# Optimization experiments

Hardware: AMD Instinct MI355X
Metric: run time of the kernel (lower is better)

## Reference

```python
import jax, jax.numpy as jnp
import numpy as np

N_TRIPLES = 2_000_000
IN_DIM = 128
FILTERS = 128
NUM_SEGMENTS = 100_000
LOG2 = 0.6931471805599453

def shifted_softplus(x):
    # softplus(x) - log(2), as in SchNet/CFnet
    return jax.nn.softplus(x) - LOG2

def setup_inputs() -> dict:
    key = jax.random.key(0)
    k1, k2, k3, k4 = jax.random.split(key, 4)
    dijk = jax.random.normal(k1, (N_TRIPLES, IN_DIM), dtype=jnp.float32)
    seg_j = jnp.sort(jax.random.randint(k2, (N_TRIPLES,), 0, NUM_SEGMENTS, dtype=jnp.int32))
    W1 = jax.random.normal(k3, (IN_DIM, FILTERS), dtype=jnp.float32) * (1.0 / np.sqrt(IN_DIM))
    b1 = jnp.zeros((FILTERS,), dtype=jnp.float32)
    W2 = jax.random.normal(k4, (FILTERS, FILTERS), dtype=jnp.float32) * (1.0 / np.sqrt(FILTERS))
    b2 = jnp.zeros((FILTERS,), dtype=jnp.float32)
    return {"dijk": dijk, "seg_j": seg_j, "W1": W1, "b1": b1, "W2": W2, "b2": b2}

def reference(dijk, seg_j, W1, b1, W2, b2):
    # dense1 + shifted softplus: [n, in] @ [in, f] -> [n, f]
    h = shifted_softplus(dijk @ W1 + b1)
    # dense2 + shifted softplus: [n, f] -> [n, f]
    w_ijk = shifted_softplus(h @ W2 + b2)
    # sum-pool over segments keyed by seg_j -> [num_segments, f]
    w_ij = jax.ops.segment_sum(w_ijk, seg_j, num_segments=NUM_SEGMENTS)
    return w_ij
```

## Files before the change

kernel.cpp:

```cpp
#include <hip/hip_runtime.h>
#include <hip/hip_bf16.h>
#include <cstdint>
#include <cstddef>


typedef float  f32x4  __attribute__((ext_vector_type(4)));
typedef __bf16 bf16x8 __attribute__((ext_vector_type(8)));

typedef uint32_t u32a    __attribute__((may_alias));
typedef bf16x8   bf16x8a __attribute__((may_alias));
typedef __bf16   bf16a   __attribute__((may_alias));

static constexpr int   N_TRIPLES = 2000000;
static constexpr int   DIM       = 128;
static constexpr int   NSEG      = 100000;
static constexpr int   ROWS      = 128;
static constexpr float LOG2F_    = 0.6931471805599453f;
static constexpr float LOG2E_    = 1.4426950408889634f;

__device__ __forceinline__ float sp2_(float y) {
  float t = __builtin_amdgcn_exp2f(-__builtin_fabsf(y));
  return fmaxf(y, 0.0f) + __builtin_amdgcn_logf(1.0f + t);
}

__global__ void wt_kernel(const float* __restrict__ W1, const float* __restrict__ W2,
                          __bf16* __restrict__ WT) {
  int t = blockIdx.x * 256 + threadIdx.x;
  int k = t >> 7;
  int n = t & 127;
  WT[n * 128 + k]         = (__bf16)(W1[t] * LOG2E_);
  WT[16384 + n * 128 + k] = (__bf16)W2[t];
}

__global__ void bias_kernel(const float* __restrict__ b1, const float* __restrict__ W2,
                            const float* __restrict__ b2,
                            float* __restrict__ b1p, float* __restrict__ b2p) {
  int n = threadIdx.x;
  float s = 0.0f;
  #pragma unroll 8
  for (int k = 0; k < 128; ++k) s += W2[k * 128 + n];
  b1p[n] = b1[n] * LOG2E_;
  b2p[n] = (b2[n] - LOG2F_ * s) * LOG2E_;
}

__global__ __launch_bounds__(512, 6) void fused_kernel(
    const float* __restrict__ dijk, const int* __restrict__ seg,
    const __bf16* __restrict__ WT,
    const float* __restrict__ b1v, const float* __restrict__ b2p,
    float* __restrict__ out)
{
  __shared__ __bf16 tile[ROWS * DIM];

  const int tid  = threadIdx.x;
  const int lane = tid & 63;
  const int wave = tid >> 6;
  const int l15  = lane & 15;
  const int g    = lane >> 4;
  const int r0   = blockIdx.x * ROWS;

  char* tb = (char*)tile;

  {
    int row = tid >> 2, q = tid & 3;
    const float* src = dijk + (size_t)(r0 + row) * DIM + q * 32;
    char* dst = tb + row * 256;
    int swz = (row & 7) << 4;
    #pragma unroll
    for (int u = 0; u < 4; ++u) {
      f32x4 v0 = *(const f32x4*)(src + u * 8);
      f32x4 v1 = *(const f32x4*)(src + u * 8 + 4);
      bf16x8 t8;
      t8[0] = (__bf16)v0[0]; t8[1] = (__bf16)v0[1]; t8[2] = (__bf16)v0[2]; t8[3] = (__bf16)v0[3];
      t8[4] = (__bf16)v1[0]; t8[5] = (__bf16)v1[1]; t8[6] = (__bf16)v1[2]; t8[7] = (__bf16)v1[3];
      *(bf16x8a*)(dst + ((q * 64 + u * 16) ^ swz)) = t8;
    }
  }

  const int colw = wave * 16 + l15;
  const float bias1 = b1v[colw];
  const float bias2 = b2p[colw];

  const int  swA = (l15 & 7) << 4;
  const char* abase = tb + l15 * 256;
  uint32_t bo[4];
  #pragma unroll
  for (int ks = 0; ks < 4; ++ks) bo[ks] = (uint32_t)((ks * 64 + g * 16) ^ swA);
  uint32_t wbase[4];
  #pragma unroll
  for (int j = 0; j < 4; ++j) {
    int rj = g * 4 + j;
    wbase[j] = (uint32_t)(rj * 256 + ((colw * 2) ^ ((rj & 7) << 4)));
  }

  __syncthreads();

  f32x4 acc[8];
  {
    bf16x8 bf1[4];
    #pragma unroll
    for (int ks = 0; ks < 4; ++ks)
      bf1[ks] = *(const bf16x8*)(WT + colw * 128 + ks * 32 + g * 8);

    #pragma unroll
    for (int mt = 0; mt < 8; ++mt) acc[mt] = (f32x4){0.f, 0.f, 0.f, 0.f};
    #pragma unroll
    for (int mt = 0; mt < 8; ++mt) {
      const char* pm = abase + mt * 4096;
      #pragma unroll
      for (int ks = 0; ks < 4; ++ks) {
        bf16x8 a = *(const bf16x8a*)(pm + bo[ks]);
        acc[mt] = __builtin_amdgcn_mfma_f32_16x16x32_bf16(a, bf1[ks], acc[mt], 0, 0, 0);
      }
    }
  }

  __syncthreads();

  #pragma unroll
  for (int mt = 0; mt < 8; ++mt) {
    #pragma unroll
    for (int j = 0; j < 4; ++j) {
      float u1 = sp2_(acc[mt][j] + bias1);
      *(bf16a*)(tb + wbase[j] + mt * 4096) = (__bf16)u1;
    }
  }

  __syncthreads();

  f32x4 acc2[8];
  {
    bf16x8 bf2[4];
    #pragma unroll
    for (int ks = 0; ks < 4; ++ks)
      bf2[ks] = *(const bf16x8*)(WT + 16384 + colw * 128 + ks * 32 + g * 8);

    #pragma unroll
    for (int mt = 0; mt < 8; ++mt) acc2[mt] = (f32x4){0.f, 0.f, 0.f, 0.f};
    #pragma unroll
    for (int mt = 0; mt < 8; ++mt) {
      const char* pm = abase + mt * 4096;
      #pragma unroll
      for (int ks = 0; ks < 4; ++ks) {
        bf16x8 a = *(const bf16x8a*)(pm + bo[ks]);
        acc2[mt] = __builtin_amdgcn_mfma_f32_16x16x32_bf16(a, bf2[ks], acc2[mt], 0, 0, 0);
      }
    }
  }

  __syncthreads();

  #pragma unroll
  for (int mt = 0; mt < 8; ++mt) {
    #pragma unroll
    for (int j = 0; j < 4; ++j) {
      float u2 = sp2_(acc2[mt][j] + bias2);
      float wv = __builtin_fmaf(u2, LOG2F_, -LOG2F_);
      *(bf16a*)(tb + wbase[j] + mt * 4096) = (__bf16)wv;
    }
  }

  __syncthreads();

  {
    const int colb = (tid & 63) * 2;
    const int hh   = tid >> 6;
    const int rbeg = hh * 16;
    const int* sp = seg + r0;
    const char* rp[8];
    #pragma unroll
    for (int k = 0; k < 8; ++k)
      rp[k] = tb + rbeg * 256 + ((colb * 2) ^ (k << 4));
    float a0 = 0.0f, a1 = 0.0f;
    int cur = sp[rbeg];
    #pragma unroll
    for (int i = 0; i < 16; ++i) {
      int s = sp[rbeg + i];
      if (s != cur) {
        atomicAdd(out + (size_t)cur * DIM + colb,     a0);
        atomicAdd(out + (size_t)cur * DIM + colb + 1, a1);
        a0 = 0.0f; a1 = 0.0f; cur = s;
      }
      uint32_t w = *(const u32a*)(rp[i & 7] + i * 256);
      a0 += __uint_as_float(w << 16);
      a1 += __uint_as_float(w & 0xffff0000u);
    }
    atomicAdd(out + (size_t)cur * DIM + colb,     a0);
    atomicAdd(out + (size_t)cur * DIM + colb + 1, a1);
  }
}

extern "C" void kernel_launch(void* const* d_in, const int* in_sizes, int n_in,
                              void* d_out, int out_size, void* d_ws, size_t ws_size,
                              hipStream_t stream) {
  const float* dijk = (const float*)d_in[0];
  const int*   seg  = (const int*)d_in[1];
  const float* W1   = (const float*)d_in[2];
  const float* b1   = (const float*)d_in[3];
  const float* W2   = (const float*)d_in[4];
  const float* b2   = (const float*)d_in[5];
  float* out = (float*)d_out;

  float*  b1p = (float*)d_ws;
  float*  b2p = (float*)((char*)d_ws + 512);
  __bf16* WT  = (__bf16*)((char*)d_ws + 1024);

  (void)hipMemsetAsync(out, 0, (size_t)NSEG * DIM * sizeof(float), stream);

  wt_kernel<<<64, 256, 0, stream>>>(W1, W2, WT);
  bias_kernel<<<1, 128, 0, stream>>>(b1, W2, b2, b1p, b2p);

  fused_kernel<<<N_TRIPLES / ROWS, 512, 0, stream>>>(dijk, seg, WT, b1p, b2p, out);
}
```

Before: 422.7 us.

## Split row tile into two halves and software-pipeline loads, GEMMs and activations

Splits the 128-row tile into two 64-row halves in shared memory. Each stage is interleaved across the halves: the second half's global load overlaps the first half's GEMM1, and each half's softplus epilogue overlaps the other half's MFMA work. The goal is to hide global-load latency and transcendental ALU time behind matrix instructions within one block. In exchange it adds two extra block barriers and reloads the W1 fragment, and register pressure may rise because several accumulator sets are live together.

After: 425.1 us. No clear change (+0.6%).

```diff
diff --git a/kernel.cpp b/kernel.cpp
--- a/kernel.cpp
+++ b/kernel.cpp
@@ -58,30 +58,24 @@
   const int g    = lane >> 4;
   const int r0   = blockIdx.x * ROWS;
 
-  char* tb = (char*)tile;
-
-  {
-    int row = tid >> 2, q = tid & 3;
-    const float* src = dijk + (size_t)(r0 + row) * DIM + q * 32;
-    char* dst = tb + row * 256;
-    int swz = (row & 7) << 4;
-    #pragma unroll
-    for (int u = 0; u < 4; ++u) {
-      f32x4 v0 = *(const f32x4*)(src + u * 8);
-      f32x4 v1 = *(const f32x4*)(src + u * 8 + 4);
-      bf16x8 t8;
-      t8[0] = (__bf16)v0[0]; t8[1] = (__bf16)v0[1]; t8[2] = (__bf16)v0[2]; t8[3] = (__bf16)v0[3];
-      t8[4] = (__bf16)v1[0]; t8[5] = (__bf16)v1[1]; t8[6] = (__bf16)v1[2]; t8[7] = (__bf16)v1[3];
-      *(bf16x8a*)(dst + ((q * 64 + u * 16) ^ swz)) = t8;
-    }
-  }
+  char* tA = (char*)tile;
+  char* tB = (char*)tile + 16384;
+
+  const int  srow = tid >> 3;
+  const int  soct = tid & 7;
+  const int  sswz = (srow & 7) << 4;
+  char* sdstA = tA + srow * 256;
+  char* sdstB = tB + srow * 256;
+  const uint32_t so0 = (uint32_t)((soct * 32)      ^ sswz);
+  const uint32_t so1 = (uint32_t)((soct * 32 + 16) ^ sswz);
+  const float* gsrcA = dijk + (size_t)(r0 + srow) * DIM + soct * 16;
+  const float* gsrcB = gsrcA + (size_t)64 * DIM;
 
   const int colw = wave * 16 + l15;
   const float bias1 = b1v[colw];
   const float bias2 = b2p[colw];
 
   const int  swA = (l15 & 7) << 4;
-  const char* abase = tb + l15 * 256;
   uint32_t bo[4];
   #pragma unroll
   for (int ks = 0; ks < 4; ++ks) bo[ks] = (uint32_t)((ks * 64 + g * 16) ^ swA);
@@ -92,84 +86,158 @@
     wbase[j] = (uint32_t)(rj * 256 + ((colw * 2) ^ ((rj & 7) << 4)));
   }
 
-  __syncthreads();
-
-  f32x4 acc[8];
-  {
+  {
+    f32x4 v0 = *(const f32x4*)(gsrcA);
+    f32x4 v1 = *(const f32x4*)(gsrcA + 4);
+    f32x4 v2 = *(const f32x4*)(gsrcA + 8);
+    f32x4 v3 = *(const f32x4*)(gsrcA + 12);
+    bf16x8 t8a, t8b;
+    t8a[0]=(__bf16)v0[0]; t8a[1]=(__bf16)v0[1]; t8a[2]=(__bf16)v0[2]; t8a[3]=(__bf16)v0[3];
+    t8a[4]=(__bf16)v1[0]; t8a[5]=(__bf16)v1[1]; t8a[6]=(__bf16)v1[2]; t8a[7]=(__bf16)v1[3];
+    t8b[0]=(__bf16)v2[0]; t8b[1]=(__bf16)v2[1]; t8b[2]=(__bf16)v2[2]; t8b[3]=(__bf16)v2[3];
+    t8b[4]=(__bf16)v3[0]; t8b[5]=(__bf16)v3[1]; t8b[6]=(__bf16)v3[2]; t8b[7]=(__bf16)v3[3];
+    *(bf16x8a*)(sdstA + so0) = t8a;
+    *(bf16x8a*)(sdstA + so1) = t8b;
+  }
+  __syncthreads();
+
+  f32x4 accA[4];
+  {
+    f32x4 v0 = *(const f32x4*)(gsrcB);
+    f32x4 v1 = *(const f32x4*)(gsrcB + 4);
+    f32x4 v2 = *(const f32x4*)(gsrcB + 8);
+    f32x4 v3 = *(const f32x4*)(gsrcB + 12);
+
     bf16x8 bf1[4];
     #pragma unroll
     for (int ks = 0; ks < 4; ++ks)
       bf1[ks] = *(const bf16x8*)(WT + colw * 128 + ks * 32 + g * 8);
 
     #pragma unroll
-    for (int mt = 0; mt < 8; ++mt) acc[mt] = (f32x4){0.f, 0.f, 0.f, 0.f};
-    #pragma unroll
-    for (int mt = 0; mt < 8; ++mt) {
-      const char* pm = abase + mt * 4096;
-      #pragma unroll
-      for (int ks = 0; ks < 4; ++ks) {
-        bf16x8 a = *(const bf16x8a*)(pm + bo[ks]);
-        acc[mt] = __builtin_amdgcn_mfma_f32_16x16x32_bf16(a, bf1[ks], acc[mt], 0, 0, 0);
-      }
-    }
-  }
-
-  __syncthreads();
-
-  #pragma unroll
-  for (int mt = 0; mt < 8; ++mt) {
-    #pragma unroll
-    for (int j = 0; j < 4; ++j) {
-      float u1 = sp2_(acc[mt][j] + bias1);
-      *(bf16a*)(tb + wbase[j] + mt * 4096) = (__bf16)u1;
-    }
-  }
-
-  __syncthreads();
-
-  f32x4 acc2[8];
-  {
-    bf16x8 bf2[4];
+    for (int mt = 0; mt < 4; ++mt) accA[mt] = (f32x4){0.f, 0.f, 0.f, 0.f};
+    #pragma unroll
+    for (int mt = 0; mt < 4; ++mt) {
+      const char* pm = tA + l15 * 256 + mt * 4096;
+      #pragma unroll
+      for (int ks = 0; ks < 4; ++ks) {
+        bf16x8 a = *(const bf16x8a*)(pm + bo[ks]);
+        accA[mt] = __builtin_amdgcn_mfma_f32_16x16x32_bf16(a, bf1[ks], accA[mt], 0, 0, 0);
+      }
+    }
+
+    bf16x8 t8a, t8b;
+    t8a[0]=(__bf16)v0[0]; t8a[1]=(__bf16)v0[1]; t8a[2]=(__bf16)v0[2]; t8a[3]=(__bf16)v0[3];
+    t8a[4]=(__bf16)v1[0]; t8a[5]=(__bf16)v1[1]; t8a[6]=(__bf16)v1[2]; t8a[7]=(__bf16)v1[3];
+    t8b[0]=(__bf16)v2[0]; t8b[1]=(__bf16)v2[1]; t8b[2]=(__bf16)v2[2]; t8b[3]=(__bf16)v2[3];
+    t8b[4]=(__bf16)v3[0]; t8b[5]=(__bf16)v3[1]; t8b[6]=(__bf16)v3[2]; t8b[7]=(__bf16)v3[3];
+    *(bf16x8a*)(sdstB + so0) = t8a;
+    *(bf16x8a*)(sdstB + so1) = t8b;
+  }
+  __syncthreads();
+
+  f32x4 accB[4];
+  {
+    bf16x8 bf1[4];
+    #pragma unroll
+    for (int ks = 0; ks < 4; ++ks)
+      bf1[ks] = *(const bf16x8*)(WT + colw * 128 + ks * 32 + g * 8);
+    #pragma unroll
+    for (int mt = 0; mt < 4; ++mt) accB[mt] = (f32x4){0.f, 0.f, 0.f, 0.f};
+    #pragma unroll
+    for (int mt = 0; mt < 4; ++mt) {
+      const char* pm = tB + l15 * 256 + mt * 4096;
+      #pragma unroll
+      for (int ks = 0; ks < 4; ++ks) {
+        bf16x8 a = *(const bf16x8a*)(pm + bo[ks]);
+        accB[mt] = __builtin_amdgcn_mfma_f32_16x16x32_bf16(a, bf1[ks], accB[mt], 0, 0, 0);
+      }
+    }
+    #pragma unroll
+    for (int mt = 0; mt < 4; ++mt) {
+      #pragma unroll
+      for (int j = 0; j < 4; ++j) {
+        float u1 = sp2_(accA[mt][j] + bias1);
+        *(bf16a*)(tA + wbase[j] + mt * 4096) = (__bf16)u1;
+      }
+    }
+  }
+  __syncthreads();
+
+  f32x4 acc2A[4];
+  bf16x8 bf2[4];
+  {
     #pragma unroll
     for (int ks = 0; ks < 4; ++ks)
       bf2[ks] = *(const bf16x8*)(WT + 16384 + colw * 128 + ks * 32 + g * 8);
-
-    #pragma unroll
-    for (int mt = 0; mt < 8; ++mt) acc2[mt] = (f32x4){0.f, 0.f, 0.f, 0.f};
-    #pragma unroll
-    for (int mt = 0; mt < 8; ++mt) {
-      const char* pm = abase + mt * 4096;
-      #pragma unroll
-      for (int ks = 0; ks < 4; ++ks) {
-        bf16x8 a = *(const bf16x8a*)(pm + bo[ks]);
-        acc2[mt] = __builtin_amdgcn_mfma_f32_16x16x32_bf16(a, bf2[ks], acc2[mt], 0, 0, 0);
-      }
-    }
-  }
-
+    #pragma unroll
+    for (int mt = 0; mt < 4; ++mt) acc2A[mt] = (f32x4){0.f, 0.f, 0.f, 0.f};
+    #pragma unroll
+    for (int mt = 0; mt < 4; ++mt) {
+      const char* pm = tA + l15 * 256 + mt * 4096;
+      #pragma unroll
+      for (int ks = 0; ks < 4; ++ks) {
+        bf16x8 a = *(const bf16x8a*)(pm + bo[ks]);
+        acc2A[mt] = __builtin_amdgcn_mfma_f32_16x16x32_bf16(a, bf2[ks], acc2A[mt], 0, 0, 0);
+      }
+    }
+    #pragma unroll
+    for (int mt = 0; mt < 4; ++mt) {
+      #pragma unroll
+      for (int j = 0; j < 4; ++j) {
+        float u1 = sp2_(accB[mt][j] + bias1);
+        *(bf16a*)(tB + wbase[j] + mt * 4096) = (__bf16)u1;
+      }
+    }
+  }
+  __syncthreads();
+
+  f32x4 acc2B[4];
+  {
+    #pragma unroll
+    for (int mt = 0; mt < 4; ++mt) acc2B[mt] = (f32x4){0.f, 0.f, 0.f, 0.f};
+    #pragma unroll
+    for (int mt = 0; mt < 4; ++mt) {
+      const char* pm = tB + l15 * 256 + mt * 4096;
+      #pragma unroll
+      for (int ks = 0; ks < 4; ++ks) {
+        bf16x8 a = *(const bf16x8a*)(pm + bo[ks]);
+        acc2B[mt] = __builtin_amdgcn_mfma_f32_16x16x32_bf16(a, bf2[ks], acc2B[mt], 0, 0, 0);
+      }
+    }
+    #pragma unroll
+    for (int mt = 0; mt < 4; ++mt) {
+      #pragma unroll
+      for (int j = 0; j < 4; ++j) {
+        float u2 = sp2_(acc2A[mt][j] + bias2);
+        float wv = __builtin_fmaf(u2, LOG2F_, -LOG2F_);
+        *(bf16a*)(tA + wbase[j] + mt * 4096) = (__bf16)wv;
+      }
+    }
+  }
   __syncthreads();
 
   #pragma unroll
-  for (int mt = 0; mt < 8; ++mt) {
+  for (int mt = 0; mt < 4; ++mt) {
     #pragma unroll
     for (int j = 0; j < 4; ++j) {
-      float u2 = sp2_(acc2[mt][j] + bias2);
+      float u2 = sp2_(acc2B[mt][j] + bias2);
       float wv = __builtin_fmaf(u2, LOG2F_, -LOG2F_);
-      *(bf16a*)(tb + wbase[j] + mt * 4096) = (__bf16)wv;
-    }
-  }
-
+      *(bf16a*)(tB + wbase[j] + mt * 4096) = (__bf16)wv;
+    }
+  }
   __syncthreads();
 
   {
     const int colb = (tid & 63) * 2;
     const int hh   = tid >> 6;
+    char* rb = (hh < 4) ? tA : tB;
+    const int rloc = (hh & 3) * 16;
     const int rbeg = hh * 16;
     const int* sp = seg + r0;
     const char* rp[8];
     #pragma unroll
     for (int k = 0; k < 8; ++k)
-      rp[k] = tb + rbeg * 256 + ((colb * 2) ^ (k << 4));
+      rp[k] = rb + rloc * 256 + ((colb * 2) ^ (k << 4));
     float a0 = 0.0f, a1 = 0.0f;
     int cur = sp[rbeg];
     #pragma unroll
```

## Switch MLP matmuls to 32x32x16 MFMA with 2x4 wave tiling and 16-row swizzle

Applied to the files above, without the earlier changes.

Replaces the 16x16x32 MFMA tiling, where each wave owned 16 columns across all 128 rows, with 32x32x16 MFMAs. Each wave now owns a 64-row by 32-column tile held in two 16-wide accumulators. The LDS XOR swizzle widens from 8 to 16 rows to match the new access patterns, and the output write-back and segment-reduction read addressing are updated to the same swizzle. The aim is fewer A-operand LDS reads per MFMA and fewer instructions. In exchange, accumulator registers per wave rise and the layout and index math become more involved.

New measurement: 515.6 us. 22.0% more time.

```diff
diff --git a/kernel.cpp b/kernel.cpp
--- a/kernel.cpp
+++ b/kernel.cpp
@@ -5,6 +5,7 @@
 
 
 typedef float  f32x4  __attribute__((ext_vector_type(4)));
+typedef float  f32x16 __attribute__((ext_vector_type(16)));
 typedef __bf16 bf16x8 __attribute__((ext_vector_type(8)));
 
 typedef uint32_t u32a    __attribute__((may_alias));
@@ -54,8 +55,10 @@
   const int tid  = threadIdx.x;
   const int lane = tid & 63;
   const int wave = tid >> 6;
-  const int l15  = lane & 15;
-  const int g    = lane >> 4;
+  const int l31  = lane & 31;
+  const int h5   = lane >> 5;
+  const int cs   = wave & 3;
+  const int rh   = wave >> 2;
   const int r0   = blockIdx.x * ROWS;
 
   char* tb = (char*)tile;
@@ -64,7 +67,7 @@
     int row = tid >> 2, q = tid & 3;
     const float* src = dijk + (size_t)(r0 + row) * DIM + q * 32;
     char* dst = tb + row * 256;
-    int swz = (row & 7) << 4;
+    int swz = (row & 15) << 4;
     #pragma unroll
     for (int u = 0; u < 4; ++u) {
       f32x4 v0 = *(const f32x4*)(src + u * 8);
@@ -76,87 +79,94 @@
     }
   }
 
-  const int colw = wave * 16 + l15;
+  const int colw = cs * 32 + l31;
   const float bias1 = b1v[colw];
   const float bias2 = b2p[colw];
 
-  const int  swA = (l15 & 7) << 4;
-  const char* abase = tb + l15 * 256;
-  uint32_t bo[4];
-  #pragma unroll
-  for (int ks = 0; ks < 4; ++ks) bo[ks] = (uint32_t)((ks * 64 + g * 16) ^ swA);
-  uint32_t wbase[4];
-  #pragma unroll
-  for (int j = 0; j < 4; ++j) {
-    int rj = g * 4 + j;
-    wbase[j] = (uint32_t)(rj * 256 + ((colw * 2) ^ ((rj & 7) << 4)));
-  }
-
-  __syncthreads();
-
-  f32x4 acc[8];
-  {
-    bf16x8 bf1[4];
-    #pragma unroll
-    for (int ks = 0; ks < 4; ++ks)
-      bf1[ks] = *(const bf16x8*)(WT + colw * 128 + ks * 32 + g * 8);
-
-    #pragma unroll
-    for (int mt = 0; mt < 8; ++mt) acc[mt] = (f32x4){0.f, 0.f, 0.f, 0.f};
-    #pragma unroll
-    for (int mt = 0; mt < 8; ++mt) {
-      const char* pm = abase + mt * 4096;
+  const int  swzA = (l31 & 15) << 4;
+  const char* abase = tb + (rh * 64 + l31) * 256;
+  uint32_t bo[8];
+  #pragma unroll
+  for (int ks = 0; ks < 8; ++ks) bo[ks] = (uint32_t)((ks * 32 + h5 * 16) ^ swzA);
+  const uint32_t wrow0 = (uint32_t)((rh * 64 + 4 * h5) * 256);
+  uint32_t e0[4];
+  #pragma unroll
+  for (int j = 0; j < 4; ++j)
+    e0[j] = (uint32_t)((colw * 2) ^ ((4 * h5 + j) << 4));
+
+  __syncthreads();
+
+  f32x16 acc0 = {}, acc1 = {};
+  #pragma unroll
+  for (int ksh = 0; ksh < 2; ++ksh) {
+    bf16x8 bf[4];
+    #pragma unroll
+    for (int i = 0; i < 4; ++i)
+      bf[i] = *(const bf16x8*)(WT + colw * 128 + (ksh * 4 + i) * 16 + h5 * 8);
+    #pragma unroll
+    for (int i = 0; i < 4; ++i) {
+      bf16x8 a0 = *(const bf16x8a*)(abase + bo[ksh * 4 + i]);
+      bf16x8 a1 = *(const bf16x8a*)(abase + 8192 + bo[ksh * 4 + i]);
+      acc0 = __builtin_amdgcn_mfma_f32_32x32x16_bf16(a0, bf[i], acc0, 0, 0, 0);
+      acc1 = __builtin_amdgcn_mfma_f32_32x32x16_bf16(a1, bf[i], acc1, 0, 0, 0);
+    }
+  }
+
+  __syncthreads();
+
+  {
+    auto spstore1 = [&](const f32x16& a, uint32_t tof) {
       #pragma unroll
-      for (int ks = 0; ks < 4; ++ks) {
-        bf16x8 a = *(const bf16x8a*)(pm + bo[ks]);
-        acc[mt] = __builtin_amdgcn_mfma_f32_16x16x32_bf16(a, bf1[ks], acc[mt], 0, 0, 0);
+      for (int q = 0; q < 4; ++q) {
+        #pragma unroll
+        for (int j = 0; j < 4; ++j) {
+          float u1 = sp2_(a[q * 4 + j] + bias1);
+          uint32_t off = wrow0 + tof + (uint32_t)(q * 2048 + j * 256)
+                       + (e0[j] ^ ((uint32_t)(q & 1) << 7));
+          *(bf16a*)(tb + off) = (__bf16)u1;
+        }
       }
-    }
-  }
-
-  __syncthreads();
-
-  #pragma unroll
-  for (int mt = 0; mt < 8; ++mt) {
-    #pragma unroll
-    for (int j = 0; j < 4; ++j) {
-      float u1 = sp2_(acc[mt][j] + bias1);
-      *(bf16a*)(tb + wbase[j] + mt * 4096) = (__bf16)u1;
-    }
-  }
-
-  __syncthreads();
-
-  f32x4 acc2[8];
-  {
-    bf16x8 bf2[4];
-    #pragma unroll
-    for (int ks = 0; ks < 4; ++ks)
-      bf2[ks] = *(const bf16x8*)(WT + 16384 + colw * 128 + ks * 32 + g * 8);
-
-    #pragma unroll
-    for (int mt = 0; mt < 8; ++mt) acc2[mt] = (f32x4){0.f, 0.f, 0.f, 0.f};
-    #pragma unroll
-    for (int mt = 0; mt < 8; ++mt) {
-      const char* pm = abase + mt * 4096;
+    };
+    spstore1(acc0, 0);
+    spstore1(acc1, 8192);
+  }
+
+  __syncthreads();
+
+  acc0 = (f32x16){}; acc1 = (f32x16){};
+  #pragma unroll
+  for (int ksh = 0; ksh < 2; ++ksh) {
+    bf16x8 bf[4];
+    #pragma unroll
+    for (int i = 0; i < 4; ++i)
+      bf[i] = *(const bf16x8*)(WT + 16384 + colw * 128 + (ksh * 4 + i) * 16 + h5 * 8);
+    #pragma unroll
+    for (int i = 0; i < 4; ++i) {
+      bf16x8 a0 = *(const bf16x8a*)(abase + bo[ksh * 4 + i]);
+      bf16x8 a1 = *(const bf16x8a*)(abase + 8192 + bo[ksh * 4 + i]);
+      acc0 = __builtin_amdgcn_mfma_f32_32x32x16_bf16(a0, bf[i], acc0, 0, 0, 0);
+      acc1 = __builtin_amdgcn_mfma_f32_32x32x16_bf16(a1, bf[i], acc1, 0, 0, 0);
+    }
+  }
+
+  __syncthreads();
+
+  {
+    auto spstore2 = [&](const f32x16& a, uint32_t tof) {
       #pragma unroll
-      for (int ks = 0; ks < 4; ++ks) {
-        bf16x8 a = *(const bf16x8a*)(pm + bo[ks]);
-        acc2[mt] = __builtin_amdgcn_mfma_f32_16x16x32_bf16(a, bf2[ks], acc2[mt], 0, 0, 0);
+      for (int q = 0; q < 4; ++q) {
+        #pragma unroll
+        for (int j = 0; j < 4; ++j) {
+          float u2 = sp2_(a[q * 4 + j] + bias2);
+          float wv = __builtin_fmaf(u2, LOG2F_, -LOG2F_);
+          uint32_t off = wrow0 + tof + (uint32_t)(q * 2048 + j * 256)
+                       + (e0[j] ^ ((uint32_t)(q & 1) << 7));
+          *(bf16a*)(tb + off) = (__bf16)wv;
+        }
       }
-    }
-  }
-
-  __syncthreads();
-
-  #pragma unroll
-  for (int mt = 0; mt < 8; ++mt) {
-    #pragma unroll
-    for (int j = 0; j < 4; ++j) {
-      float u2 = sp2_(acc2[mt][j] + bias2);
-      float wv = __builtin_fmaf(u2, LOG2F_, -LOG2F_);
-      *(bf16a*)(tb + wbase[j] + mt * 4096) = (__bf16)wv;
-    }
+    };
+    spstore2(acc0, 0);
+    spstore2(acc1, 8192);
   }
 
   __syncthreads();
@@ -166,10 +176,8 @@
     const int hh   = tid >> 6;
     const int rbeg = hh * 16;
     const int* sp = seg + r0;
-    const char* rp[8];
-    #pragma unroll
-    for (int k = 0; k < 8; ++k)
-      rp[k] = tb + rbeg * 256 + ((colb * 2) ^ (k << 4));
+    const char* rbase = tb + rbeg * 256;
+    const uint32_t cx = (uint32_t)(colb * 2);
     float a0 = 0.0f, a1 = 0.0f;
     int cur = sp[rbeg];
     #pragma unroll
@@ -180,7 +188,7 @@
         atomicAdd(out + (size_t)cur * DIM + colb + 1, a1);
         a0 = 0.0f; a1 = 0.0f; cur = s;
       }
-      uint32_t w = *(const u32a*)(rp[i & 7] + i * 256);
+      uint32_t w = *(const u32a*)(rbase + i * 256 + (cx ^ (uint32_t)(i << 4)));
       a0 += __uint_as_float(w << 16);
       a1 += __uint_as_float(w & 0xffff0000u);
     }
```
